# Kernel optimization log

Measured on AMD Instinct MI355X. Metric: run time of the kernel, lower is better.

Reference implementation:

```python
import jax, jax.numpy as jnp
import numpy as np

B, T, H = 4, 2048, 1024
NH = 16
HD = H // NH  # 64
FF = 4 * H


def setup_inputs() -> dict:
    key = jax.random.key(0)
    ks = jax.random.split(key, 11)
    s = 0.02
    return {
        "x": jax.random.normal(ks[0], (B, T, H), dtype=jnp.float32),
        "Wq": jax.random.normal(ks[1], (H, H), dtype=jnp.float32) * s,
        "bq": jnp.zeros((H,), dtype=jnp.float32),
        "Wk": jax.random.normal(ks[2], (H, H), dtype=jnp.float32) * s,
        "bk": jnp.zeros((H,), dtype=jnp.float32),
        "Wv": jax.random.normal(ks[3], (H, H), dtype=jnp.float32) * s,
        "bv": jnp.zeros((H,), dtype=jnp.float32),
        "W1": jax.random.normal(ks[4], (H, FF), dtype=jnp.float32) * s,
        "b1": jnp.zeros((FF,), dtype=jnp.float32),
        "W2": jax.random.normal(ks[5], (FF, H), dtype=jnp.float32) * s,
        "b2": jnp.zeros((H,), dtype=jnp.float32),
    }


def _block(x, Wq, bq, Wk, bk, Wv, bv, W1, b1, W2, b2):
    b, t, h = x.shape
    # multi-head masked self-attention; NOTE: scale = full h_dim ** 0.5 (as in source)
    q = (x @ Wq + bq).reshape(b, t, NH, HD).transpose(0, 2, 1, 3)  # [B,nH,T,HD]
    k = (x @ Wk + bk).reshape(b, t, NH, HD).transpose(0, 2, 1, 3)
    v = (x @ Wv + bv).reshape(b, t, NH, HD).transpose(0, 2, 1, 3)
    att = jnp.einsum("bnqd,bnkd->bnqk", q, k) / (h ** 0.5)  # [B,nH,T,T]
    causal = jnp.tril(jnp.ones((t, t), dtype=bool))
    att = jnp.where(causal, att, -jnp.inf)
    w = jax.nn.softmax(att, axis=-1)
    attn_out = jnp.einsum("bnqk,bnkd->bnqd", w, v).transpose(0, 2, 1, 3).reshape(b, t, h)
    x = x + attn_out
    # MLP (dropout p=0 -> identity)
    mlp = jax.nn.gelu(x @ W1 + b1) @ W2 + b2
    return x + mlp


def reference(x, Wq, bq, Wk, bk, Wv, bv, W1, b1, W2, b2):
    return _block(x, Wq, bq, Wk, bk, Wv, bv, W1, b1, W2, b2)
```

## Files before the change

### kernel.cpp

```cpp
#include <hip/hip_runtime.h>
#include <cstdint>
#include <cstddef>

typedef unsigned short u16;
typedef __attribute__((ext_vector_type(8))) __bf16 bf16x8;
typedef __attribute__((ext_vector_type(4))) __bf16 bf16x4;
typedef __attribute__((ext_vector_type(4))) float f32x4;
typedef __attribute__((ext_vector_type(4))) u16 u16x4;

#define MFMA(a, b, c) __builtin_amdgcn_mfma_f32_16x16x32_bf16((a), (b), (c), 0, 0, 0)

__device__ __forceinline__ u16 f2b(float f) {
  union { __bf16 h; u16 u; } v;
  v.h = (__bf16)f;
  return v.u;
}

__device__ __forceinline__ void gld16(const void* g, void* l) {
  __builtin_amdgcn_global_load_lds(
      (__attribute__((address_space(1))) void*)(void*)(g),
      (__attribute__((address_space(3))) void*)(l), 16, 0, 0);
}

__device__ __forceinline__ size_t qk_off(int t, int hd) {
  return (size_t)((((t >> 4) * 2 + (hd >> 5)) * 512)
                  + ((((hd >> 3) & 3) * 16 + (t & 15)) * 8) + (hd & 7));
}
__device__ __forceinline__ size_t v_off(int t, int hd) {
  int kk = ((t & 15) << 2) | ((t >> 4) & 3);
  return (size_t)(((t >> 6) * 4096)
                  + (((hd >> 4) * 2 + (kk >> 5)) * 512)
                  + ((((kk >> 3) & 3) * 16 + (hd & 15)) * 8) + (kk & 7));
}

__global__ void xconv(const float* __restrict__ in, u16* __restrict__ out, int n) {
  int i = (blockIdx.x * blockDim.x + threadIdx.x) * 4;
  if (i >= n) return;
  float4 v = *(const float4*)(in + i);
  u16x4 o;
  o[0] = f2b(v.x); o[1] = f2b(v.y); o[2] = f2b(v.z); o[3] = f2b(v.w);
  *(u16x4*)(out + i) = o;
}

__global__ void wtrans_all(const float* __restrict__ Wq, const float* __restrict__ Wk,
                           const float* __restrict__ Wv, const float* __restrict__ W1,
                           const float* __restrict__ W2, u16* __restrict__ Wqkvt,
                           u16* __restrict__ W1t, u16* __restrict__ W2t) {
  __shared__ float tile[32][33];
  int blk = blockIdx.x;
  const float* W;
  u16* Wt;
  int Kd, Nd, nx;
  if (blk < 3072) {
    int s = blk >> 10;
    blk &= 1023;
    W = (s == 0) ? Wq : (s == 1) ? Wk : Wv;
    Wt = Wqkvt + (size_t)s * 1048576;
    Kd = 1024; Nd = 1024; nx = 32;
  } else if (blk < 7168) {
    blk -= 3072; W = W1; Wt = W1t; Kd = 1024; Nd = 4096; nx = 128;
  } else {
    blk -= 7168; W = W2; Wt = W2t; Kd = 4096; Nd = 1024; nx = 32;
  }
  int n0 = (blk % nx) * 32, k0 = (blk / nx) * 32;
  int tx = threadIdx.x, ty = threadIdx.y;
#pragma unroll
  for (int i = 0; i < 4; i++)
    tile[ty + i * 8][tx] = W[(size_t)(k0 + ty + i * 8) * Nd + n0 + tx];
  __syncthreads();
#pragma unroll
  for (int i = 0; i < 4; i++)
    Wt[(size_t)(n0 + ty + i * 8) * Kd + k0 + tx] = f2b(tile[tx][ty + i * 8]);
}

template <int MODE>
__global__ __launch_bounds__(512, 2) void gemm_big(
    const u16* __restrict__ A, const u16* __restrict__ Bt,
    const float* __restrict__ b0, void* __restrict__ outp,
    int N, int K) {
  __shared__ __attribute__((aligned(16))) u16 As_[2][16384];
  __shared__ __attribute__((aligned(16))) u16 Bs_[2][16384];
  const int tid = threadIdx.x;
  const int wid = tid >> 6, lane = tid & 63;
  const int g = lane >> 4, r = lane & 15;

  const int xcd = blockIdx.x & 7;
  const int ii = blockIdx.x >> 3;
  const int c4 = ii >> 4, w = ii & 15;
  const int bm = xcd * 4 + (w >> 2);
  const int bn = c4 * 4 + (w & 3);

  const int wrow = (wid >> 2) * 128;
  const int wcol = (wid & 3) * 64;

  const int ko0 = ((0 * 4 + g) ^ (r & 7)) * 8;
  const int ko1 = ((1 * 4 + g) ^ (r & 7)) * 8;

  size_t aOff[4], bOff[4];
#pragma unroll
  for (int i4 = 0; i4 < 4; i4++) {
    int cc = i4 * 512 + tid, row = cc >> 3;
    int js = ((cc & 7) ^ (row & 7)) * 8;
    aOff[i4] = (size_t)(bm * 256 + row) * K + js;
    bOff[i4] = (size_t)(bn * 256 + row) * K + js;
  }

  f32x4 acc[8][4];
  const f32x4 zero4 = {0.f, 0.f, 0.f, 0.f};
#pragma unroll
  for (int i = 0; i < 8; i++)
#pragma unroll
    for (int j = 0; j < 4; j++) acc[i][j] = zero4;

#pragma unroll
  for (int i4 = 0; i4 < 4; i4++) {
    gld16(A + aOff[i4], &As_[0][(i4 * 512 + tid) * 8]);
    gld16(Bt + bOff[i4], &Bs_[0][(i4 * 512 + tid) * 8]);
  }
  asm volatile("s_waitcnt vmcnt(0)" ::: "memory");
  __builtin_amdgcn_s_barrier();

  const int KT = K >> 6;
  int cur = 0;
  for (int t = 0; t < KT; ++t) {
    const u16* as = As_[cur];
    const u16* bs = Bs_[cur];
    const int nxt = cur ^ 1;
    const bool more = (t + 1) < KT;
    const size_t k1 = (size_t)(t + 1) * 64;

    if (more) {
#pragma unroll
      for (int i4 = 0; i4 < 4; i4++)
        gld16(A + aOff[i4] + k1, &As_[nxt][(i4 * 512 + tid) * 8]);
    }

    {
      bf16x8 af[8], bf[4];
#pragma unroll
      for (int mt = 0; mt < 8; mt++)
        af[mt] = *(const bf16x8*)&as[(wrow + mt * 16 + r) * 64 + ko0];
#pragma unroll
      for (int nt = 0; nt < 4; nt++)
        bf[nt] = *(const bf16x8*)&bs[(wcol + nt * 16 + r) * 64 + ko0];
#pragma unroll
      for (int mt = 0; mt < 8; mt++)
#pragma unroll
        for (int nt = 0; nt < 4; nt++)
          acc[mt][nt] = MFMA(af[mt], bf[nt], acc[mt][nt]);
    }

    if (more) {
#pragma unroll
      for (int i4 = 0; i4 < 4; i4++)
        gld16(Bt + bOff[i4] + k1, &Bs_[nxt][(i4 * 512 + tid) * 8]);
    }

    {
      bf16x8 af[8], bf[4];
#pragma unroll
      for (int mt = 0; mt < 8; mt++)
        af[mt] = *(const bf16x8*)&as[(wrow + mt * 16 + r) * 64 + ko1];
#pragma unroll
      for (int nt = 0; nt < 4; nt++)
        bf[nt] = *(const bf16x8*)&bs[(wcol + nt * 16 + r) * 64 + ko1];
#pragma unroll
      for (int mt = 0; mt < 8; mt++)
#pragma unroll
        for (int nt = 0; nt < 4; nt++)
          acc[mt][nt] = MFMA(af[mt], bf[nt], acc[mt][nt]);
    }

    if (more) {
      asm volatile("s_waitcnt vmcnt(0)" ::: "memory");
      __builtin_amdgcn_s_barrier();
    }
    cur = nxt;
  }

#pragma unroll
  for (int mt = 0; mt < 8; mt++) {
#pragma unroll
    for (int nt = 0; nt < 4; nt++) {
      int col = bn * 256 + wcol + nt * 16 + r;
      float bv = b0[col];
#pragma unroll
      for (int q = 0; q < 4; q++) {
        int row = bm * 256 + wrow + mt * 16 + g * 4 + q;
        float v = acc[mt][nt][q] + bv;
        if (MODE == 2) {
          const float c1 = -2.3025850929940457f;
          const float c2 = c1 * 0.044715f;
          float t2 = v * v;
          float z = v * (c1 + c2 * t2);
          float sg = 1.0f / (1.0f + __builtin_amdgcn_exp2f(z));
          ((u16*)outp)[(size_t)row * N + col] = f2b(v * sg);
        }
      }
    }
  }
}

template <int MODE>
__global__ __launch_bounds__(512, 2) void gemm256(
    const u16* __restrict__ A, const u16* __restrict__ Bt,
    const float* __restrict__ b0, const float* __restrict__ b1,
    const float* __restrict__ b2, void* __restrict__ outp,
    const float* __restrict__ resid, int N, int K, float scale) {
  __shared__ __attribute__((aligned(16))) u16 As_[3][16384];
  __shared__ __attribute__((aligned(16))) u16 Bs_[3][8192];
  const int tid = threadIdx.x;
  const int wid = tid >> 6, lane = tid & 63;
  const int g = lane >> 4, r = lane & 15;

  const int xcd = blockIdx.x & 7;
  const int ii = blockIdx.x >> 3;
  const int bm = xcd * 4 + ((ii & 31) >> 3);
  const int bn = (ii >> 5) * 8 + (ii & 7);

  const int wrow = (wid >> 1) * 64;
  const int wcol = (wid & 1) * 64;

  const int ko0 = ((0 * 4 + g) ^ (r & 7)) * 8;
  const int ko1 = ((1 * 4 + g) ^ (r & 7)) * 8;

  size_t aOff[4], bOff[2];
#pragma unroll
  for (int i4 = 0; i4 < 4; i4++) {
    int cc = i4 * 512 + tid, row = cc >> 3;
    int js = ((cc & 7) ^ (row & 7)) * 8;
    aOff[i4] = (size_t)(bm * 256 + row) * K + js;
  }
#pragma unroll
  for (int i2 = 0; i2 < 2; i2++) {
    int cc = i2 * 512 + tid, row = cc >> 3;
    int js = ((cc & 7) ^ (row & 7)) * 8;
    bOff[i2] = (size_t)(bn * 128 + row) * K + js;
  }

  f32x4 acc[4][4];
  const f32x4 zero4 = {0.f, 0.f, 0.f, 0.f};
#pragma unroll
  for (int i = 0; i < 4; i++)
#pragma unroll
    for (int j = 0; j < 4; j++) acc[i][j] = zero4;

#pragma unroll
  for (int i4 = 0; i4 < 4; i4++) gld16(A + aOff[i4], &As_[0][(i4 * 512 + tid) * 8]);
#pragma unroll
  for (int i2 = 0; i2 < 2; i2++) gld16(Bt + bOff[i2], &Bs_[0][(i2 * 512 + tid) * 8]);
#pragma unroll
  for (int i4 = 0; i4 < 4; i4++) gld16(A + aOff[i4] + 64, &As_[1][(i4 * 512 + tid) * 8]);
#pragma unroll
  for (int i2 = 0; i2 < 2; i2++) gld16(Bt + bOff[i2] + 64, &Bs_[1][(i2 * 512 + tid) * 8]);
  asm volatile("s_waitcnt vmcnt(6)" ::: "memory");
  __builtin_amdgcn_s_barrier();

  const int KT = K >> 6;
  int cur = 0;
  for (int t = 0; t < KT; ++t) {
    const u16* as = As_[cur];
    const u16* bs = Bs_[cur];
    const int stg = (cur == 0) ? 2 : cur - 1;
    const bool more = (t + 2) < KT;
    const size_t k2 = (size_t)(t + 2) * 64;

    bf16x8 af0[4], bf0[4], af1[4], bf1[4];
#pragma unroll
    for (int mt = 0; mt < 4; mt++) {
      af0[mt] = *(const bf16x8*)&as[(wrow + mt * 16 + r) * 64 + ko0];
      af1[mt] = *(const bf16x8*)&as[(wrow + mt * 16 + r) * 64 + ko1];
    }
#pragma unroll
    for (int nt = 0; nt < 4; nt++) {
      bf0[nt] = *(const bf16x8*)&bs[(wcol + nt * 16 + r) * 64 + ko0];
      bf1[nt] = *(const bf16x8*)&bs[(wcol + nt * 16 + r) * 64 + ko1];
    }

    if (more) {
#pragma unroll
      for (int i4 = 0; i4 < 4; i4++)
        gld16(A + aOff[i4] + k2, &As_[stg][(i4 * 512 + tid) * 8]);
#pragma unroll
      for (int i2 = 0; i2 < 2; i2++)
        gld16(Bt + bOff[i2] + k2, &Bs_[stg][(i2 * 512 + tid) * 8]);
    }

#pragma unroll
    for (int mt = 0; mt < 4; mt++)
#pragma unroll
      for (int nt = 0; nt < 4; nt++)
        acc[mt][nt] = MFMA(af0[mt], bf0[nt], acc[mt][nt]);
#pragma unroll
    for (int mt = 0; mt < 4; mt++)
#pragma unroll
      for (int nt = 0; nt < 4; nt++)
        acc[mt][nt] = MFMA(af1[mt], bf1[nt], acc[mt][nt]);

    if (t + 1 < KT) {
      if (more) asm volatile("s_waitcnt vmcnt(6)" ::: "memory");
      else      asm volatile("s_waitcnt vmcnt(0)" ::: "memory");
    }
    __builtin_amdgcn_s_barrier();
    cur = (cur == 2) ? 0 : cur + 1;
  }

#pragma unroll
  for (int mt = 0; mt < 4; mt++) {
#pragma unroll
    for (int nt = 0; nt < 4; nt++) {
      int col = bn * 128 + wcol + nt * 16 + r;
      float bv;
      if (MODE == 4) {
        int sec = col >> 10, hcol = col & 1023;
        bv = (sec == 0) ? b0[hcol] : (sec == 1) ? b1[hcol] : b2[hcol];
      } else {
        bv = b0[col];
      }
#pragma unroll
      for (int q = 0; q < 4; q++) {
        int row = bm * 256 + wrow + mt * 16 + g * 4 + q;
        float v = acc[mt][nt][q] + bv;
        if (MODE == 3) {
          ((float*)outp)[(size_t)row * N + col] = v + resid[(size_t)row * N + col];
        } else if (MODE == 4) {
          int sec = col >> 10, hcol = col & 1023;
          int head = hcol >> 6, hd = hcol & 63;
          int bb = row >> 11, tt = row & 2047;
          size_t hbase = ((size_t)bb * 16 + head) * 131072;
          u16* qout = (u16*)outp;
          if (sec == 0) {
            qout[hbase + qk_off(tt, hd)] = f2b(v * scale);
          } else if (sec == 1) {
            (qout + 8388608)[hbase + qk_off(tt, hd)] = f2b(v);
          } else {
            (qout + 16777216)[hbase + v_off(tt, hd)] = f2b(v);
          }
        }
      }
    }
  }
}

__global__ __launch_bounds__(256) void attn_kernel(
    const u16* __restrict__ Q, const u16* __restrict__ Kc,
    const u16* __restrict__ Vt, const float* __restrict__ x,
    float* __restrict__ x1, u16* __restrict__ xb1) {
  const int bh = blockIdx.x & 63;
  const int slot = blockIdx.x >> 6;
  const int tid = threadIdx.x;
  const int wid = tid >> 6, lane = tid & 63;
  const int g = lane >> 4, c = lane & 15;
  const u16* Qh = Q + (size_t)bh * 131072;
  const u16* Kh = Kc + (size_t)bh * 131072;
  const u16* Vh = Vt + (size_t)bh * 131072;
  const int b = bh >> 4, head = bh & 15;

  __shared__ __attribute__((aligned(16))) u16 Ks[8192];
  __shared__ __attribute__((aligned(16))) u16 Vs[8192];
  __shared__ __attribute__((aligned(16))) u16 P[4][32][72];

  bf16x8 ones;
#pragma unroll
  for (int i = 0; i < 8; i++) ones[i] = (__bf16)1.0f;

  const f32x4 zero4 = {0.f, 0.f, 0.f, 0.f};

  for (int phase = 0; phase < 2; ++phase) {
    const int bt = phase ? (15 - slot) : slot;
    const int q0b = bt * 128;
    const int q0 = q0b + wid * 32;
    const int kendw = q0 + 32;
    const int nkt = bt + 1;

    bf16x8 qf[2][2];
#pragma unroll
    for (int mt = 0; mt < 2; mt++)
#pragma unroll
      for (int h = 0; h < 2; h++)
        qf[mt][h] = *(const bf16x8*)&Qh[(((q0 >> 4) + mt) * 2 + h) * 512 + lane * 8];

    f32x4 o[2][4];
    f32x4 lac[2];
#pragma unroll
    for (int mt = 0; mt < 2; mt++) {
      lac[mt] = zero4;
#pragma unroll
      for (int i = 0; i < 4; i++) o[mt][i] = zero4;
    }

    for (int kt = 0; kt < nkt; ++kt) {
      const int k0 = kt * 128;
#pragma unroll
      for (int r2 = 0; r2 < 4; r2++) {
        int idx = (r2 * 256 + tid) * 8;
        gld16(Kh + (size_t)k0 * 64 + idx, Ks + idx);
        gld16(Vh + (size_t)k0 * 64 + idx, Vs + idx);
      }
      __syncthreads();

#pragma unroll
      for (int s2 = 0; s2 < 2; ++s2) {
        const int k0s = k0 + s2 * 64;
        if (k0s < kendw) {
          bf16x8 kf[4][2], vf[4][2];
#pragma unroll
          for (int nt = 0; nt < 4; nt++)
#pragma unroll
            for (int h = 0; h < 2; h++) {
              kf[nt][h] = *(const bf16x8*)&Ks[s2 * 4096 + (nt * 2 + h) * 512 + lane * 8];
              vf[nt][h] = *(const bf16x8*)&Vs[s2 * 4096 + (nt * 2 + h) * 512 + lane * 8];
            }

          f32x4 sv[2][4];
#pragma unroll
          for (int mt = 0; mt < 2; mt++)
#pragma unroll
            for (int nt = 0; nt < 4; nt++) sv[mt][nt] = zero4;
#pragma unroll
          for (int nt = 0; nt < 4; nt++)
#pragma unroll
            for (int mt = 0; mt < 2; mt++) {
              sv[mt][nt] = MFMA(qf[mt][0], kf[nt][0], sv[mt][nt]);
              sv[mt][nt] = MFMA(qf[mt][1], kf[nt][1], sv[mt][nt]);
            }

          if (k0s + 64 > q0) {
#pragma unroll
            for (int mt = 0; mt < 2; mt++)
#pragma unroll
              for (int rr = 0; rr < 4; rr++) {
                int q = q0 + mt * 16 + g * 4 + rr;
#pragma unroll
                for (int nt = 0; nt < 4; nt++)
                  if (k0s + nt * 16 + c > q) sv[mt][nt][rr] = -1e30f;
              }
          }

#pragma unroll
          for (int mt = 0; mt < 2; mt++)
#pragma unroll
            for (int rr = 0; rr < 4; rr++) {
              union { u16x4 u; bf16x4 h; } pw;
#pragma unroll
              for (int nt = 0; nt < 4; nt++)
                pw.h[nt] = (__bf16)__builtin_amdgcn_exp2f(sv[mt][nt][rr]);
              *(u16x4*)&P[wid][mt * 16 + g * 4 + rr][4 * c] = pw.u;
            }

          asm volatile("s_waitcnt lgkmcnt(0)" ::: "memory");

#pragma unroll
          for (int mt = 0; mt < 2; mt++) {
            bf16x8 pf0 = *(const bf16x8*)&P[wid][mt * 16 + c][g * 8];
            bf16x8 pf1 = *(const bf16x8*)&P[wid][mt * 16 + c][32 + g * 8];
            lac[mt] = MFMA(pf0, ones, lac[mt]);
            lac[mt] = MFMA(pf1, ones, lac[mt]);
#pragma unroll
            for (int ot = 0; ot < 4; ot++) {
              f32x4 oo = MFMA(pf0, vf[ot][0], o[mt][ot]);
              o[mt][ot] = MFMA(pf1, vf[ot][1], oo);
            }
          }
        }
      }
      __syncthreads();
    }

    float inv[2][4];
#pragma unroll
    for (int mt = 0; mt < 2; mt++)
#pragma unroll
      for (int rr = 0; rr < 4; rr++) inv[mt][rr] = 1.0f / lac[mt][rr];
#pragma unroll
    for (int mt = 0; mt < 2; mt++)
#pragma unroll
      for (int ot = 0; ot < 4; ot++)
#pragma unroll
        for (int rr = 0; rr < 4; rr++) {
          int t = q0 + mt * 16 + g * 4 + rr;
          int hd = ot * 16 + c;
          size_t xi = ((size_t)b * 2048 + t) * 1024 + head * 64 + hd;
          float v = x[xi] + o[mt][ot][rr] * inv[mt][rr];
          x1[xi] = v;
          xb1[xi] = f2b(v);
        }
  }
}

extern "C" void kernel_launch(void* const* d_in, const int* in_sizes, int n_in,
                              void* d_out, int out_size, void* d_ws, size_t ws_size,
                              hipStream_t stream) {
  (void)in_sizes; (void)n_in; (void)out_size; (void)ws_size;
  const float* x = (const float*)d_in[0];
  const float* Wq = (const float*)d_in[1];
  const float* bq = (const float*)d_in[2];
  const float* Wk = (const float*)d_in[3];
  const float* bk = (const float*)d_in[4];
  const float* Wv = (const float*)d_in[5];
  const float* bv = (const float*)d_in[6];
  const float* W1 = (const float*)d_in[7];
  const float* b1 = (const float*)d_in[8];
  const float* W2 = (const float*)d_in[9];
  const float* b2 = (const float*)d_in[10];

  char* ws = (char*)d_ws;
  size_t off = 0;
  auto alloc = [&](size_t bytes) {
    char* p = ws + off;
    off += (bytes + 255) & ~(size_t)255;
    return p;
  };
  u16* xb    = (u16*)alloc(8192ull * 1024 * 2);
  u16* Wqkvt = (u16*)alloc(3072ull * 1024 * 2);
  u16* W1t   = (u16*)alloc(4096ull * 1024 * 2);
  u16* W2t   = (u16*)alloc(1024ull * 4096 * 2);
  u16* Qb    = (u16*)alloc(3ull * 8192 * 1024 * 2);
  float* x1  = (float*)alloc(8192ull * 1024 * 4);
  u16* hb    = (u16*)alloc(8192ull * 4096 * 2);
  u16* xb1   = xb;
  u16* Kb    = Qb + 8388608;
  u16* Vtb   = Qb + 16777216;

  const float qscale = 1.4426950408889634f / 32.0f;

  xconv<<<dim3(8192), dim3(256), 0, stream>>>(x, xb, 8192 * 1024);
  wtrans_all<<<dim3(11264), dim3(32, 8), 0, stream>>>(
      Wq, Wk, Wv, W1, W2, Wqkvt, W1t, W2t);
  gemm256<4><<<dim3(768), dim3(512), 0, stream>>>(
      xb, Wqkvt, bq, bk, bv, Qb, nullptr, 3072, 1024, qscale);
  attn_kernel<<<dim3(512), dim3(256), 0, stream>>>(Qb, Kb, Vtb, x, x1, xb1);
  gemm_big<2><<<dim3(512), dim3(512), 0, stream>>>(
      xb1, W1t, b1, hb, 4096, 1024);
  gemm256<3><<<dim3(256), dim3(512), 0, stream>>>(
      hb, W2t, b2, nullptr, nullptr, d_out, x1, 1024, 4096, 1.0f);
}
```

Baseline: 430.7 us.

## Restructure W1 GEMM into 8-wave quadrant ping-pong pipeline with staged loads

Rewrites the FFN up-projection GEMM main loop so each wave computes four 64x32 quadrant sub-tiles. Global-to-LDS loads for the next K-tiles are split into half-tile chunks interleaved between the quadrant phases. Barriers, s_setprio and sched_barrier fence the LDS fragment reads from the MFMA bursts, aiming to keep the matrix units busy while memory traffic overlaps. This adds many more barriers per iteration and depends on exact vmcnt accounting for correctness.

```diff
diff --git a/kernel.cpp b/kernel.cpp
--- a/kernel.cpp
+++ b/kernel.cpp
@@ -74,7 +74,7 @@
 }
 
 template <int MODE>
-__global__ __launch_bounds__(512, 2) void gemm_big(
+__global__ __launch_bounds__(512, 2) void gemm8p(
     const u16* __restrict__ A, const u16* __restrict__ Bt,
     const float* __restrict__ b0, void* __restrict__ outp,
     int N, int K) {
@@ -90,8 +90,8 @@
   const int bm = xcd * 4 + (w >> 2);
   const int bn = c4 * 4 + (w & 3);
 
-  const int wrow = (wid >> 2) * 128;
-  const int wcol = (wid & 3) * 64;
+  const int mrow = (wid >> 2) * 64;
+  const int ncol = (wid & 3) * 32;
 
   const int ko0 = ((0 * 4 + g) ^ (r & 7)) * 8;
   const int ko1 = ((1 * 4 + g) ^ (r & 7)) * 8;
@@ -117,77 +117,129 @@
     gld16(A + aOff[i4], &As_[0][(i4 * 512 + tid) * 8]);
     gld16(Bt + bOff[i4], &Bs_[0][(i4 * 512 + tid) * 8]);
   }
-  asm volatile("s_waitcnt vmcnt(0)" ::: "memory");
+  gld16(A + aOff[0] + 64, &As_[1][(0 * 512 + tid) * 8]);
+  gld16(A + aOff[1] + 64, &As_[1][(1 * 512 + tid) * 8]);
+  gld16(Bt + bOff[2] + 64, &Bs_[1][(2 * 512 + tid) * 8]);
+  gld16(Bt + bOff[3] + 64, &Bs_[1][(3 * 512 + tid) * 8]);
+  asm volatile("s_waitcnt vmcnt(4)" ::: "memory");
   __builtin_amdgcn_s_barrier();
 
   const int KT = K >> 6;
-  int cur = 0;
   for (int t = 0; t < KT; ++t) {
-    const u16* as = As_[cur];
-    const u16* bs = Bs_[cur];
-    const int nxt = cur ^ 1;
-    const bool more = (t + 1) < KT;
-    const size_t k1 = (size_t)(t + 1) * 64;
-
-    if (more) {
-#pragma unroll
-      for (int i4 = 0; i4 < 4; i4++)
-        gld16(A + aOff[i4] + k1, &As_[nxt][(i4 * 512 + tid) * 8]);
-    }
-
-    {
-      bf16x8 af[8], bf[4];
-#pragma unroll
-      for (int mt = 0; mt < 8; mt++)
-        af[mt] = *(const bf16x8*)&as[(wrow + mt * 16 + r) * 64 + ko0];
-#pragma unroll
-      for (int nt = 0; nt < 4; nt++)
-        bf[nt] = *(const bf16x8*)&bs[(wcol + nt * 16 + r) * 64 + ko0];
-#pragma unroll
-      for (int mt = 0; mt < 8; mt++)
-#pragma unroll
-        for (int nt = 0; nt < 4; nt++)
-          acc[mt][nt] = MFMA(af[mt], bf[nt], acc[mt][nt]);
-    }
-
-    if (more) {
-#pragma unroll
-      for (int i4 = 0; i4 < 4; i4++)
-        gld16(Bt + bOff[i4] + k1, &Bs_[nxt][(i4 * 512 + tid) * 8]);
-    }
-
-    {
-      bf16x8 af[8], bf[4];
-#pragma unroll
-      for (int mt = 0; mt < 8; mt++)
-        af[mt] = *(const bf16x8*)&as[(wrow + mt * 16 + r) * 64 + ko1];
-#pragma unroll
-      for (int nt = 0; nt < 4; nt++)
-        bf[nt] = *(const bf16x8*)&bs[(wcol + nt * 16 + r) * 64 + ko1];
-#pragma unroll
-      for (int mt = 0; mt < 8; mt++)
-#pragma unroll
-        for (int nt = 0; nt < 4; nt++)
-          acc[mt][nt] = MFMA(af[mt], bf[nt], acc[mt][nt]);
-    }
-
-    if (more) {
-      asm volatile("s_waitcnt vmcnt(0)" ::: "memory");
-      __builtin_amdgcn_s_barrier();
-    }
-    cur = nxt;
-  }
-
-#pragma unroll
-  for (int mt = 0; mt < 8; mt++) {
-#pragma unroll
-    for (int nt = 0; nt < 4; nt++) {
-      int col = bn * 256 + wcol + nt * 16 + r;
+    const int p = t & 1, pn = p ^ 1;
+    const u16* as = As_[p];
+    const u16* bs = Bs_[p];
+    const bool m1 = (t + 1) < KT, m2 = (t + 2) < KT;
+    const size_t k1 = (size_t)(t + 1) * 64, k2 = (size_t)(t + 2) * 64;
+    bf16x8 af[4][2], bf[2][2];
+
+#pragma unroll
+    for (int mt = 0; mt < 4; mt++) {
+      int rw = mrow + mt * 16 + r;
+      af[mt][0] = *(const bf16x8*)&as[rw * 64 + ko0];
+      af[mt][1] = *(const bf16x8*)&as[rw * 64 + ko1];
+    }
+#pragma unroll
+    for (int nt = 0; nt < 2; nt++) {
+      int rw = ncol + nt * 16 + r;
+      bf[nt][0] = *(const bf16x8*)&bs[rw * 64 + ko0];
+      bf[nt][1] = *(const bf16x8*)&bs[rw * 64 + ko1];
+    }
+    if (m1) {
+      gld16(A + aOff[2] + k1, &As_[pn][(1024 + tid) * 8]);
+      gld16(A + aOff[3] + k1, &As_[pn][(1536 + tid) * 8]);
+    }
+    __builtin_amdgcn_s_barrier();
+    asm volatile("s_waitcnt lgkmcnt(0)" ::: "memory");
+    __builtin_amdgcn_sched_barrier(0);
+    __builtin_amdgcn_s_setprio(1);
+#pragma unroll
+    for (int mt = 0; mt < 4; mt++)
+#pragma unroll
+      for (int nt = 0; nt < 2; nt++)
+        acc[mt][nt] = MFMA(af[mt][1], bf[nt][1], MFMA(af[mt][0], bf[nt][0], acc[mt][nt]));
+    __builtin_amdgcn_s_setprio(0);
+    __builtin_amdgcn_s_barrier();
+
+#pragma unroll
+    for (int nt = 0; nt < 2; nt++) {
+      int rw = 128 + ncol + nt * 16 + r;
+      bf[nt][0] = *(const bf16x8*)&bs[rw * 64 + ko0];
+      bf[nt][1] = *(const bf16x8*)&bs[rw * 64 + ko1];
+    }
+    if (m1) {
+      gld16(Bt + bOff[0] + k1, &Bs_[pn][(tid) * 8]);
+      gld16(Bt + bOff[1] + k1, &Bs_[pn][(512 + tid) * 8]);
+    }
+    __builtin_amdgcn_s_barrier();
+    asm volatile("s_waitcnt lgkmcnt(0)" ::: "memory");
+    __builtin_amdgcn_sched_barrier(0);
+    __builtin_amdgcn_s_setprio(1);
+#pragma unroll
+    for (int mt = 0; mt < 4; mt++)
+#pragma unroll
+      for (int nt = 0; nt < 2; nt++)
+        acc[mt][2 + nt] = MFMA(af[mt][1], bf[nt][1], MFMA(af[mt][0], bf[nt][0], acc[mt][2 + nt]));
+    __builtin_amdgcn_s_setprio(0);
+    __builtin_amdgcn_s_barrier();
+
+#pragma unroll
+    for (int mt = 0; mt < 4; mt++) {
+      int rw = 128 + mrow + mt * 16 + r;
+      af[mt][0] = *(const bf16x8*)&as[rw * 64 + ko0];
+      af[mt][1] = *(const bf16x8*)&as[rw * 64 + ko1];
+    }
+    if (m2) {
+      gld16(A + aOff[0] + k2, &As_[p][(tid) * 8]);
+      gld16(A + aOff[1] + k2, &As_[p][(512 + tid) * 8]);
+    }
+    __builtin_amdgcn_s_barrier();
+    asm volatile("s_waitcnt lgkmcnt(0)" ::: "memory");
+    __builtin_amdgcn_sched_barrier(0);
+    __builtin_amdgcn_s_setprio(1);
+#pragma unroll
+    for (int mt = 0; mt < 4; mt++)
+#pragma unroll
+      for (int nt = 0; nt < 2; nt++)
+        acc[4 + mt][2 + nt] = MFMA(af[mt][1], bf[nt][1], MFMA(af[mt][0], bf[nt][0], acc[4 + mt][2 + nt]));
+    __builtin_amdgcn_s_setprio(0);
+    __builtin_amdgcn_s_barrier();
+
+#pragma unroll
+    for (int nt = 0; nt < 2; nt++) {
+      int rw = ncol + nt * 16 + r;
+      bf[nt][0] = *(const bf16x8*)&bs[rw * 64 + ko0];
+      bf[nt][1] = *(const bf16x8*)&bs[rw * 64 + ko1];
+    }
+    if (m2) {
+      gld16(Bt + bOff[2] + k2, &Bs_[p][(1024 + tid) * 8]);
+      gld16(Bt + bOff[3] + k2, &Bs_[p][(1536 + tid) * 8]);
+    }
+    __builtin_amdgcn_s_barrier();
+    asm volatile("s_waitcnt lgkmcnt(0)" ::: "memory");
+    __builtin_amdgcn_sched_barrier(0);
+    __builtin_amdgcn_s_setprio(1);
+#pragma unroll
+    for (int mt = 0; mt < 4; mt++)
+#pragma unroll
+      for (int nt = 0; nt < 2; nt++)
+        acc[4 + mt][nt] = MFMA(af[mt][1], bf[nt][1], MFMA(af[mt][0], bf[nt][0], acc[4 + mt][nt]));
+    __builtin_amdgcn_s_setprio(0);
+    if (m2) asm volatile("s_waitcnt vmcnt(4)" ::: "memory");
+    else    asm volatile("s_waitcnt vmcnt(0)" ::: "memory");
+    __builtin_amdgcn_s_barrier();
+  }
+
+#pragma unroll
+  for (int am = 0; am < 8; am++) {
+#pragma unroll
+    for (int an = 0; an < 4; an++) {
+      int col = bn * 256 + (an >> 1) * 128 + ncol + (an & 1) * 16 + r;
       float bv = b0[col];
 #pragma unroll
       for (int q = 0; q < 4; q++) {
-        int row = bm * 256 + wrow + mt * 16 + g * 4 + q;
-        float v = acc[mt][nt][q] + bv;
+        int row = bm * 256 + (am >> 2) * 128 + mrow + (am & 3) * 16 + g * 4 + q;
+        float v = acc[am][an][q] + bv;
         if (MODE == 2) {
           const float c1 = -2.3025850929940457f;
           const float c2 = c1 * 0.044715f;
@@ -530,7 +582,7 @@
   gemm256<4><<<dim3(768), dim3(512), 0, stream>>>(
       xb, Wqkvt, bq, bk, bv, Qb, nullptr, 3072, 1024, qscale);
   attn_kernel<<<dim3(512), dim3(256), 0, stream>>>(Qb, Kb, Vtb, x, x1, xb1);
-  gemm_big<2><<<dim3(512), dim3(512), 0, stream>>>(
+  gemm8p<2><<<dim3(512), dim3(512), 0, stream>>>(
       xb1, W1t, b1, hb, 4096, 1024);
   gemm256<3><<<dim3(256), dim3(512), 0, stream>>>(
       hb, W2t, b2, nullptr, nullptr, d_out, x1, 1024, 4096, 1.0f);
```

New measurement: 425.5 us. No clear change (-1.2%).
